# Kernel tuning notes

Measured on AMD Instinct MI355X. Metric: run time of the kernel, lower is better.

Reference implementation:

```python
import jax, jax.numpy as jnp
import numpy as np

E, H = 1024, 16
D = E // H


def softmax_1(x):
    # softmax_1: exp(x_i) / (1 + sum_j exp(x_j)), computed stably
    m = jnp.max(x, axis=-1, keepdims=True)
    e = jnp.exp(x - m)
    return e / (jnp.exp(-m) + jnp.sum(e, axis=-1, keepdims=True))


def setup_inputs() -> dict:
    key = jax.random.key(0)
    ks = jax.random.split(key, 8)
    S, B = 1024, 4
    x = jax.random.normal(ks[0], (S, B, E), dtype=jnp.float32)
    attn_bias = jax.random.normal(ks[1], (B, H, S, S), dtype=jnp.float32)
    attn_bias_mul = jax.random.uniform(ks[2], (B, H, S, S), dtype=jnp.float32)
    key_padding_mask = jax.random.randint(ks[3], (B, S), 0, 2).astype(jnp.bool_)
    # xavier-ish init for linear layers (torch Linear: y = x @ W.T + b)
    W_in = jax.random.normal(ks[4], (3 * E, E), dtype=jnp.float32) * (E ** -0.5)
    b_in = jnp.zeros((3 * E,), dtype=jnp.float32)
    W_out = jax.random.normal(ks[5], (E, E), dtype=jnp.float32) * (E ** -0.5)
    b_out = jnp.zeros((E,), dtype=jnp.float32)
    return {"x": x, "attn_bias": attn_bias, "attn_bias_mul": attn_bias_mul,
            "key_padding_mask": key_padding_mask,
            "W_in": W_in, "b_in": b_in, "W_out": W_out, "b_out": b_out}


def reference(x, attn_bias, attn_bias_mul, key_padding_mask, W_in, b_in, W_out, b_out):
    S, B, _ = x.shape
    # in_proj -> [S, B, 3E] -> [B*H, S, 3D]
    qkv = x @ W_in.T + b_in
    qkv = qkv.reshape(S, B * H, 3 * D).transpose(1, 0, 2)
    q, k, v = jnp.split(qkv, 3, axis=-1)
    q = q * (D ** -0.5)
    # scores [B*H, S, S] with additive bias
    aw = jnp.einsum('bqd,bkd->bqk', q, k) + attn_bias.reshape(B * H, S, S)
    # key padding mask (dropout p=0 -> identity)
    kpm = key_padding_mask[:, None, None, :]  # [B,1,1,S]
    aw = jnp.where(kpm, -jnp.inf, aw.reshape(B, H, S, S)).reshape(B * H, S, S)
    abm = jnp.where(kpm, 0.0, attn_bias_mul).reshape(B * H, S, S)
    p = softmax_1(aw) * abm
    attn = jnp.einsum('bqk,bkd->bqd', p, v)  # [B*H, S, D]
    attn = attn.transpose(1, 0, 2).reshape(S, B, E)
    return attn @ W_out.T + b_out
```

## Files before the change

kernel.cpp:

```cpp
#include <hip/hip_runtime.h>
#include <stdint.h>
#include <stddef.h>

typedef __attribute__((ext_vector_type(4))) float f32x4;
typedef __attribute__((ext_vector_type(4))) int   i32x4;
typedef __attribute__((ext_vector_type(8))) short s16x8;
typedef __attribute__((ext_vector_type(4))) short s16x4;
typedef __attribute__((ext_vector_type(8))) __bf16 bf16x8;

#define AS3 __attribute__((address_space(3)))
#define AS1 __attribute__((address_space(1)))

__device__ inline void gload16(const void* g, void* l) {
  __builtin_amdgcn_global_load_lds((AS1 const void*)g, (AS3 void*)l, 16, 0, 0);
}

__device__ inline f32x4 mfma16(s16x8 a, s16x8 b, f32x4 c) {
  return __builtin_amdgcn_mfma_f32_16x16x32_bf16(
      __builtin_bit_cast(bf16x8, a), __builtin_bit_cast(bf16x8, b), c, 0, 0, 0);
}

__device__ inline short f2bf(float f) {
  unsigned u = __builtin_bit_cast(unsigned, f);
  u += 0x7FFFu + ((u >> 16) & 1u);
  return (short)(u >> 16);
}
__device__ inline float bf2f(short x) {
  unsigned u = ((unsigned)(unsigned short)x) << 16;
  return __builtin_bit_cast(float, u);
}

__global__ void cast_all(const float* __restrict__ x, const float* __restrict__ wi,
                         const float* __restrict__ wo, short* __restrict__ xb,
                         short* __restrict__ wib, short* __restrict__ wob) {
  int i = blockIdx.x * 256 + threadIdx.x;
  const float* src;
  short* dst;
  int off;
  if (i < 1048576)      { src = x;  dst = xb;  off = i; }
  else if (i < 1835008) { src = wi; dst = wib; off = i - 1048576; }
  else                  { src = wo; dst = wob; off = i - 1835008; }
  f32x4 v = *(const f32x4*)(src + (size_t)off * 4);
  s16x4 o;
#pragma unroll
  for (int r = 0; r < 4; ++r) o[r] = f2bf(v[r]);
  *(s16x4*)(dst + (size_t)off * 4) = o;
}

template <int OBF, int FR>
__global__ __launch_bounds__(256, 2) void gemm_bt(
    const short* __restrict__ A, const short* __restrict__ B,
    const float* __restrict__ bias, void* __restrict__ Cv,
    int M, int N, int K) {
  const int TILE = FR * 32;
  const int tid = threadIdx.x, w = tid >> 6, lane = tid & 63;
  const int quad = lane >> 4, l15 = lane & 15;
  const int wm = w >> 1, wn = w & 1;
  const int m0 = blockIdx.y * TILE, n0 = blockIdx.x * TILE;
  __shared__ short As[TILE * 32], Bs[TILE * 32];
  f32x4 acc[FR][FR];
#pragma unroll
  for (int i = 0; i < FR; ++i)
#pragma unroll
    for (int j = 0; j < FR; ++j) acc[i][j] = (f32x4){0.f, 0.f, 0.f, 0.f};
  const int rs = lane >> 2, cs = (lane & 3) * 8;
  const int nkt = K >> 5;
  for (int kt = 0; kt < nkt; ++kt) {
    const int k0 = kt * 32;
#pragma unroll
    for (int j = 0; j < FR / 2; ++j) {
      gload16(A + (size_t)(m0 + w * (FR * 8) + j * 16 + rs) * K + k0 + cs,
              &As[w * (FR * 256) + j * 512]);
      gload16(B + (size_t)(n0 + w * (FR * 8) + j * 16 + rs) * K + k0 + cs,
              &Bs[w * (FR * 256) + j * 512]);
    }
    __syncthreads();
    s16x8 af[FR], bfr[FR];
#pragma unroll
    for (int i = 0; i < FR; ++i) {
      af[i]  = *(const s16x8*)&As[(wm * (FR * 16) + i * 16 + l15) * 32 + quad * 8];
      bfr[i] = *(const s16x8*)&Bs[(wn * (FR * 16) + i * 16 + l15) * 32 + quad * 8];
    }
#pragma unroll
    for (int ms = 0; ms < FR; ++ms)
#pragma unroll
      for (int ns = 0; ns < FR; ++ns)
        acc[ms][ns] = mfma16(af[ms], bfr[ns], acc[ms][ns]);
    __syncthreads();
  }
#pragma unroll
  for (int ms = 0; ms < FR; ++ms) {
    const int row0 = m0 + wm * (FR * 16) + ms * 16 + quad * 4;
#pragma unroll
    for (int ns = 0; ns < FR; ++ns) {
      const int col = n0 + wn * (FR * 16) + ns * 16 + l15;
      const float bv = bias[col];
#pragma unroll
      for (int r = 0; r < 4; ++r) {
        float v = acc[ms][ns][r] + bv;
        if (OBF) ((short*)Cv)[(size_t)(row0 + r) * N + col] = f2bf(v);
        else     ((float*)Cv)[(size_t)(row0 + r) * N + col] = v;
      }
    }
  }
}

__global__ void repack_all(const short* __restrict__ qkv, short* __restrict__ qh,
                           short* __restrict__ kh, short* __restrict__ vT) {
  __shared__ short t[64][80];
  const int bh = blockIdx.x, st_ = blockIdx.y;
  const int b_ = bh >> 4, h_ = bh & 15;
  const int tid = threadIdx.x;
#pragma unroll
  for (int part = 0; part < 4; ++part) {
    int lin = part * 256 + tid;
    int dg = lin & 7, ty = (lin >> 3) & 1, s_l = lin >> 4;
    int s = st_ * 64 + s_l;
    s16x8 v = *(const s16x8*)(qkv + (size_t)(s * 4 + b_) * 3072 + h_ * 192 + ty * 64 + dg * 8);
    if (ty == 0) {
#pragma unroll
      for (int i = 0; i < 8; ++i) v[i] = f2bf(bf2f(v[i]) * 0.125f);
      *(s16x8*)&qh[((size_t)bh << 16) + (size_t)s * 64 + dg * 8] = v;
    } else {
      *(s16x8*)&kh[((size_t)bh << 16) + (size_t)s * 64 + dg * 8] = v;
    }
  }
#pragma unroll
  for (int part = 0; part < 2; ++part) {
    int lin = part * 256 + tid;
    int ch = lin & 7, s_l = lin >> 3;
    int s = st_ * 64 + s_l;
    *(s16x8*)&t[s_l][ch * 8] =
        *(const s16x8*)(qkv + (size_t)(s * 4 + b_) * 3072 + h_ * 192 + 128 + ch * 8);
  }
  __syncthreads();
#pragma unroll
  for (int part = 0; part < 2; ++part) {
    int lin = part * 256 + tid;
    int sc = lin & 7, d_l = lin >> 3;
    s16x8 vv;
#pragma unroll
    for (int j = 0; j < 8; ++j) vv[j] = t[sc * 8 + j][d_l];
    *(s16x8*)&vT[((size_t)bh << 16) + (size_t)d_l * 1024 + st_ * 64 + sc * 8] = vv;
  }
}

__global__ __launch_bounds__(256, 4) void attn_fused(
    const short* __restrict__ qh, const short* __restrict__ kh,
    const short* __restrict__ vT, const float* __restrict__ bias,
    const float* __restrict__ abm, const int* __restrict__ kpm,
    short* __restrict__ attnbf) {
  const int tid = threadIdx.x;
  const int w = tid >> 6, lane = tid & 63, quad = lane >> 4, l15 = lane & 15;
  const int bh = blockIdx.x, qb = blockIdx.y;
  const int b_ = bh >> 4, h_ = bh & 15;
  const short* khd = kh + ((size_t)bh << 16);
  const short* vTd = vT + ((size_t)bh << 16);
  const int qw = qb * 64 + w * 16;
  const float* biasd = bias + ((size_t)bh << 20) + (size_t)(qw + l15) * 1024;
  const float* abmd  = abm  + ((size_t)bh << 20) + (size_t)(qw + l15) * 1024;
  const int*   kpmd  = kpm + (b_ << 10);

  __shared__ short wl[4][16 * 40];
  __shared__ float alds[4][16];

  s16x8 qf[2];
#pragma unroll
  for (int t = 0; t < 2; ++t)
    qf[t] = *(const s16x8*)&qh[((size_t)bh << 16) + (size_t)(qw + l15) * 64 + t * 32 + quad * 8];

  f32x4 o[4];
#pragma unroll
  for (int ds = 0; ds < 4; ++ds) o[ds] = (f32x4){0.f, 0.f, 0.f, 0.f};
  float mrun = -1e30f, lrun = 0.f;

  struct Pack { f32x4 bs[2]; f32x4 ab[2]; i32x4 kp[2]; };
  Pack P0, P1;

  auto loadP = [&](int kt, Pack& P) {
    const int kb = kt * 32;
#pragma unroll
    for (int ms = 0; ms < 2; ++ms) {
      P.bs[ms] = *(const f32x4*)&biasd[kb + ms * 16 + quad * 4];
      P.ab[ms] = *(const f32x4*)&abmd [kb + ms * 16 + quad * 4];
      P.kp[ms] = *(const i32x4*)&kpmd[kb + ms * 16 + quad * 4];
    }
  };

  auto compute = [&](int kt, Pack& P) {
    const int kb = kt * 32;
    const f32x4 z4 = {0.f, 0.f, 0.f, 0.f};
    s16x8 vf[4];
#pragma unroll
    for (int ds = 0; ds < 4; ++ds)
      vf[ds] = *(const s16x8*)&vTd[(size_t)(ds * 16 + l15) * 1024 + kb + quad * 8];
    f32x4 st[2];
#pragma unroll
    for (int ms = 0; ms < 2; ++ms) {
      s16x8 a0 = *(const s16x8*)&khd[(size_t)(kb + ms * 16 + l15) * 64 + quad * 8];
      s16x8 a1 = *(const s16x8*)&khd[(size_t)(kb + ms * 16 + l15) * 64 + 32 + quad * 8];
      st[ms] = mfma16(a1, qf[1], mfma16(a0, qf[0], z4));
    }
    float mloc = -1e30f;
#pragma unroll
    for (int ms = 0; ms < 2; ++ms)
#pragma unroll
      for (int r = 0; r < 4; ++r) {
        float sc = st[ms][r] + P.bs[ms][r];
        sc = (P.kp[ms][r] != 0) ? -1e30f : sc;
        st[ms][r] = sc;
        mloc = fmaxf(mloc, sc);
      }
    mloc = fmaxf(mloc, __shfl_xor(mloc, 16));
    mloc = fmaxf(mloc, __shfl_xor(mloc, 32));
    float mn = fmaxf(mrun, mloc);
    float al = __expf(mrun - mn);
    mrun = mn;
    float lloc = 0.f;
#pragma unroll
    for (int ms = 0; ms < 2; ++ms)
#pragma unroll
      for (int r = 0; r < 4; ++r) {
        float e = (P.kp[ms][r] != 0) ? 0.f : __expf(st[ms][r] - mrun);
        st[ms][r] = e;
        lloc += e;
      }
    lloc += __shfl_xor(lloc, 16);
    lloc += __shfl_xor(lloc, 32);
    lrun = lrun * al + lloc;
    alds[w][l15] = al;
#pragma unroll
    for (int ms = 0; ms < 2; ++ms) {
      s16x4 pk;
#pragma unroll
      for (int r = 0; r < 4; ++r) pk[r] = f2bf(st[ms][r] * P.ab[ms][r]);
      *(s16x4*)&wl[w][l15 * 40 + ms * 16 + quad * 4] = pk;
    }
    f32x4 av = *(const f32x4*)&alds[w][quad * 4];
    s16x8 pf = *(const s16x8*)&wl[w][l15 * 40 + quad * 8];
#pragma unroll
    for (int ds = 0; ds < 4; ++ds) o[ds] *= av;
#pragma unroll
    for (int ds = 0; ds < 4; ++ds)
      o[ds] = mfma16(pf, vf[ds], o[ds]);
  };

  loadP(0, P0);
  loadP(1, P1);
  for (int kt = 0; kt < 32; kt += 2) {
    compute(kt, P0);
    if (kt + 2 < 32) loadP(kt + 2, P0);
    compute(kt + 1, P1);
    if (kt + 3 < 32) loadP(kt + 3, P1);
  }

  float rd = 1.f / (__expf(-mrun) + lrun);
  alds[w][l15] = rd;
  f32x4 rdv = *(const f32x4*)&alds[w][quad * 4];
#pragma unroll
  for (int ds = 0; ds < 4; ++ds) {
    f32x4 ov = o[ds] * rdv;
#pragma unroll
    for (int r = 0; r < 4; ++r) {
      int s = qw + quad * 4 + r;
      attnbf[(size_t)(s * 4 + b_) * 1024 + h_ * 64 + ds * 16 + l15] = f2bf(ov[r]);
    }
  }
}

extern "C" void kernel_launch(void* const* d_in, const int* in_sizes, int n_in,
                              void* d_out, int out_size, void* d_ws, size_t ws_size,
                              hipStream_t stream) {
  const float* x     = (const float*)d_in[0];
  const float* bias  = (const float*)d_in[1];
  const float* abm   = (const float*)d_in[2];
  const int*   kpm   = (const int*)  d_in[3];
  const float* W_in  = (const float*)d_in[4];
  const float* b_in  = (const float*)d_in[5];
  const float* W_out = (const float*)d_in[6];
  const float* b_out = (const float*)d_in[7];
  float* out = (float*)d_out;

  char* ws = (char*)d_ws;
  short* xbf    = (short*)(ws);
  short* wibf   = (short*)(ws + (8u << 20));
  short* wobf   = (short*)(ws + (14u << 20) + (512u << 10));
  short* qkvbf  = (short*)(ws + (16u << 20) + (768u << 10));
  short* qh     = (short*)(ws + (40u << 20) + (768u << 10));
  short* kh     = (short*)(ws + (48u << 20) + (768u << 10));
  short* vTh    = (short*)(ws + (56u << 20) + (768u << 10));
  short* attnbf = (short*)(ws + (64u << 20) + (768u << 10));

  cast_all<<<8192, 256, 0, stream>>>(x, W_in, W_out, xbf, wibf, wobf);

  gemm_bt<1, 4><<<dim3(24, 32), 256, 0, stream>>>(xbf, wibf, b_in, (void*)qkvbf,
                                                  4096, 3072, 1024);

  repack_all<<<dim3(64, 16), 256, 0, stream>>>(qkvbf, qh, kh, vTh);

  attn_fused<<<dim3(64, 16), 256, 0, stream>>>(qh, kh, vTh, bias, abm, kpm, attnbf);

  gemm_bt<0, 2><<<dim3(16, 64), 256, 0, stream>>>(attnbf, wobf, b_out, (void*)out,
                                                  4096, 1024, 1024);
}
```

Baseline: 705.7 us.

## Stage K/V tiles and key mask through LDS with async global-to-LDS pipeline

Each K and V tile is now loaded cooperatively into swizzled LDS buffers with global_load_lds, four buffers deep, instead of every wave reading them from global memory on its own. The key padding mask is copied to LDS once per block. Bias and abm register prefetch goes from two to three tiles, with manual vmcnt waits and a barrier each iteration. This aims to cut redundant global traffic and hide load latency. The cost is more LDS, a per-tile block barrier, lower occupancy (launch bounds 4 to 3), and a hand-tuned waitcnt that must match the number of loads in flight.

```diff
diff --git a/kernel.cpp b/kernel.cpp
--- a/kernel.cpp
+++ b/kernel.cpp
@@ -145,7 +145,7 @@
   }
 }
 
-__global__ __launch_bounds__(256, 4) void attn_fused(
+__global__ __launch_bounds__(256, 3) void attn_fused(
     const short* __restrict__ qh, const short* __restrict__ kh,
     const short* __restrict__ vT, const float* __restrict__ bias,
     const float* __restrict__ abm, const int* __restrict__ kpm,
@@ -154,6 +154,7 @@
   const int w = tid >> 6, lane = tid & 63, quad = lane >> 4, l15 = lane & 15;
   const int bh = blockIdx.x, qb = blockIdx.y;
   const int b_ = bh >> 4, h_ = bh & 15;
+  const short* qhd = qh + ((size_t)bh << 16);
   const short* khd = kh + ((size_t)bh << 16);
   const short* vTd = vT + ((size_t)bh << 16);
   const int qw = qb * 64 + w * 16;
@@ -161,44 +162,56 @@
   const float* abmd  = abm  + ((size_t)bh << 20) + (size_t)(qw + l15) * 1024;
   const int*   kpmd  = kpm + (b_ << 10);
 
+  __shared__ short kbuf[4][32 * 64];
+  __shared__ short vbuf[4][64 * 32];
   __shared__ short wl[4][16 * 40];
   __shared__ float alds[4][16];
+  __shared__ int   kpl[1024];
 
   s16x8 qf[2];
 #pragma unroll
   for (int t = 0; t < 2; ++t)
-    qf[t] = *(const s16x8*)&qh[((size_t)bh << 16) + (size_t)(qw + l15) * 64 + t * 32 + quad * 8];
+    qf[t] = *(const s16x8*)&qhd[(size_t)(qw + l15) * 64 + t * 32 + quad * 8];
 
   f32x4 o[4];
 #pragma unroll
   for (int ds = 0; ds < 4; ++ds) o[ds] = (f32x4){0.f, 0.f, 0.f, 0.f};
   float mrun = -1e30f, lrun = 0.f;
 
-  struct Pack { f32x4 bs[2]; f32x4 ab[2]; i32x4 kp[2]; };
-  Pack P0, P1;
-
-  auto loadP = [&](int kt, Pack& P) {
+  struct Pack { f32x4 bs[2]; f32x4 ab[2]; };
+  Pack P[3];
+
+  const int l7 = lane & 7, lr3 = lane >> 3;
+  const int l3 = lane & 3, lr2 = (lane >> 2) & 3;
+  auto stage = [&](int kt, int pb) {
+    gload16(khd + (size_t)kt * 2048 + (size_t)(w * 8 + lr3) * 64 + (size_t)(l7 ^ lr3) * 8,
+            &kbuf[pb][w * 512]);
+    gload16(vTd + (size_t)(w * 16 + (lane >> 2)) * 1024 + kt * 32 + (size_t)(l3 ^ lr2) * 8,
+            &vbuf[pb][w * 512]);
+  };
+  auto loadP = [&](int kt, Pack& Pp) {
     const int kb = kt * 32;
 #pragma unroll
     for (int ms = 0; ms < 2; ++ms) {
-      P.bs[ms] = *(const f32x4*)&biasd[kb + ms * 16 + quad * 4];
-      P.ab[ms] = *(const f32x4*)&abmd [kb + ms * 16 + quad * 4];
-      P.kp[ms] = *(const i32x4*)&kpmd[kb + ms * 16 + quad * 4];
+      Pp.bs[ms] = *(const f32x4*)&biasd[kb + ms * 16 + quad * 4];
+      Pp.ab[ms] = *(const f32x4*)&abmd [kb + ms * 16 + quad * 4];
     }
   };
 
-  auto compute = [&](int kt, Pack& P) {
+  auto compute = [&](int kt, int pb, Pack& Pp) {
     const int kb = kt * 32;
     const f32x4 z4 = {0.f, 0.f, 0.f, 0.f};
-    s16x8 vf[4];
-#pragma unroll
-    for (int ds = 0; ds < 4; ++ds)
-      vf[ds] = *(const s16x8*)&vTd[(size_t)(ds * 16 + l15) * 1024 + kb + quad * 8];
+    i32x4 kp[2];
+#pragma unroll
+    for (int ms = 0; ms < 2; ++ms)
+      kp[ms] = *(const i32x4*)&kpl[kb + ms * 16 + quad * 4];
     f32x4 st[2];
 #pragma unroll
     for (int ms = 0; ms < 2; ++ms) {
-      s16x8 a0 = *(const s16x8*)&khd[(size_t)(kb + ms * 16 + l15) * 64 + quad * 8];
-      s16x8 a1 = *(const s16x8*)&khd[(size_t)(kb + ms * 16 + l15) * 64 + 32 + quad * 8];
+      const int rK = ms * 16 + l15;
+      const int sw = rK & 7;
+      s16x8 a0 = *(const s16x8*)&kbuf[pb][rK * 64 + (quad ^ sw) * 8];
+      s16x8 a1 = *(const s16x8*)&kbuf[pb][rK * 64 + ((quad + 4) ^ sw) * 8];
       st[ms] = mfma16(a1, qf[1], mfma16(a0, qf[0], z4));
     }
     float mloc = -1e30f;
@@ -206,8 +219,8 @@
     for (int ms = 0; ms < 2; ++ms)
 #pragma unroll
       for (int r = 0; r < 4; ++r) {
-        float sc = st[ms][r] + P.bs[ms][r];
-        sc = (P.kp[ms][r] != 0) ? -1e30f : sc;
+        float sc = st[ms][r] + Pp.bs[ms][r];
+        sc = (kp[ms][r] != 0) ? -1e30f : sc;
         st[ms][r] = sc;
         mloc = fmaxf(mloc, sc);
       }
@@ -221,7 +234,7 @@
     for (int ms = 0; ms < 2; ++ms)
 #pragma unroll
       for (int r = 0; r < 4; ++r) {
-        float e = (P.kp[ms][r] != 0) ? 0.f : __expf(st[ms][r] - mrun);
+        float e = (kp[ms][r] != 0) ? 0.f : __expf(st[ms][r] - mrun);
         st[ms][r] = e;
         lloc += e;
       }
@@ -233,7 +246,7 @@
     for (int ms = 0; ms < 2; ++ms) {
       s16x4 pk;
 #pragma unroll
-      for (int r = 0; r < 4; ++r) pk[r] = f2bf(st[ms][r] * P.ab[ms][r]);
+      for (int r = 0; r < 4; ++r) pk[r] = f2bf(st[ms][r] * Pp.ab[ms][r]);
       *(s16x4*)&wl[w][l15 * 40 + ms * 16 + quad * 4] = pk;
     }
     f32x4 av = *(const f32x4*)&alds[w][quad * 4];
@@ -241,17 +254,30 @@
 #pragma unroll
     for (int ds = 0; ds < 4; ++ds) o[ds] *= av;
 #pragma unroll
-    for (int ds = 0; ds < 4; ++ds)
-      o[ds] = mfma16(pf, vf[ds], o[ds]);
+    for (int ds = 0; ds < 4; ++ds) {
+      const int rV = ds * 16 + l15;
+      s16x8 vf = *(const s16x8*)&vbuf[pb][rV * 32 + (quad ^ (rV & 3)) * 8];
+      o[ds] = mfma16(pf, vf, o[ds]);
+    }
   };
 
-  loadP(0, P0);
-  loadP(1, P1);
-  for (int kt = 0; kt < 32; kt += 2) {
-    compute(kt, P0);
-    if (kt + 2 < 32) loadP(kt + 2, P0);
-    compute(kt + 1, P1);
-    if (kt + 3 < 32) loadP(kt + 3, P1);
+  gload16(kpmd + w * 256 + lane * 4, &kpl[w * 256]);
+  stage(0, 0);
+  stage(1, 1);
+  asm volatile("" ::: "memory");
+  loadP(0, P[0]);
+  loadP(1, P[1]);
+  asm volatile("" ::: "memory");
+
+#pragma unroll
+  for (int t = 0; t < 32; ++t) {
+    const int tn = (t + 2 < 32) ? (t + 2) : 31;
+    stage(tn, (t + 2) & 3);
+    loadP(tn, P[(t + 2) % 3]);
+    asm volatile("s_waitcnt vmcnt(12)" ::: "memory");
+    __builtin_amdgcn_s_barrier();
+    asm volatile("" ::: "memory");
+    compute(t, t & 3, P[t % 3]);
   }
 
   float rd = 1.f / (__expf(-mrun) + lrun);
```

After: 657.3 us. 1.07x faster.
